# Kernel tuning notes

Hardware: AMD Instinct MI355X
Metric: run time of the kernel (lower is better)

Reference implementation:

```python
import jax, jax.numpy as jnp
import numpy as np

EPS_LAM = 1e-6
GN_GROUPS = 4
GN_EPS = 1e-5


def _conv(x, k):
    # x: (N, Cin, H, W), k: (Cout, Cin, 3, 3), SAME padding, stride 1
    return jax.lax.conv_general_dilated(x, k, (1, 1), 'SAME',
                                        dimension_numbers=('NCHW', 'OIHW', 'NCHW'))


def _clifford_conv(x, wa, wb, ba, bb):
    # Cl(0,1) (complex-style) Clifford conv: channels split into two blade components.
    C = x.shape[1]
    h = C // 2
    a, b = x[:, :h], x[:, h:]
    oa = _conv(a, wa) - _conv(b, wb) + ba[None, :, None, None]
    ob = _conv(a, wb) + _conv(b, wa) + bb[None, :, None, None]
    return jnp.concatenate([oa, ob], axis=1)


def _helmholtz(x):
    # Project the vector field (vx = first half of channels, vy = second half)
    # onto its divergence-free component in Fourier space.
    N, C, H, W = x.shape
    h = C // 2
    vx, vy = x[:, :h], x[:, h:]
    kx = jnp.fft.rfftfreq(W)[None, :]   # (1, FW)
    ky = jnp.fft.fftfreq(H)[:, None]    # (H, 1)
    k2 = kx * kx + ky * ky              # (H, FW)
    vxh = jnp.fft.rfft2(vx, norm='ortho')
    vyh = jnp.fft.rfft2(vy, norm='ortho')
    num = kx * vxh + ky * vyh
    p = jnp.where(k2 == 0, 0.0, num / jnp.where(k2 == 0, 1.0, k2))
    vxp = jnp.fft.irfft2(vxh - kx * p, s=(H, W), norm='ortho')
    vyp = jnp.fft.irfft2(vyh - ky * p, s=(H, W), norm='ortho')
    return jnp.concatenate([vxp, vyp], axis=1)


def _group_norm(x, w, b):
    N, C, H, W = x.shape
    xg = x.reshape(N, GN_GROUPS, -1)
    mu = xg.mean(-1, keepdims=True)
    var = xg.var(-1, keepdims=True)
    xn = ((xg - mu) * jax.lax.rsqrt(var + GN_EPS)).reshape(N, C, H, W)
    return xn * w[None, :, None, None] + b[None, :, None, None]


def setup_inputs() -> dict:
    key = jax.random.key(0)
    ks = jax.random.split(key, 6)
    B, T, C, H, W = 2, 16, 128, 64, 64
    hC = C // 2
    sc = 0.05
    return {
        'x_seq': jax.random.normal(ks[0], (B, T, C, H, W), jnp.float32),
        'dt_seq': jax.random.uniform(ks[1], (B, T), jnp.float32, 0.05, 1.0),
        'gen_w': jax.random.normal(ks[2], (C, 2 * C), jnp.float32) * (1.0 / np.sqrt(C)),
        'gen_b': jnp.zeros((2 * C,), jnp.float32),
        'cw_a': jax.random.normal(ks[3], (hC, hC, 3, 3), jnp.float32) * sc,
        'cw_b': jax.random.normal(ks[4], (hC, hC, 3, 3), jnp.float32) * sc,
        'cb_a': jnp.zeros((hC,), jnp.float32),
        'cb_b': jnp.zeros((hC,), jnp.float32),
        'gn_w': jnp.ones((C,), jnp.float32),
        'gn_b': jnp.zeros((C,), jnp.float32),
    }


def reference(x_seq, dt_seq, gen_w, gen_b, cw_a, cw_b, cb_a, cb_b, gn_w, gn_b):
    B, T, C, H, W = x_seq.shape
    dt = dt_seq[:, :, None, None, None]                   # (B,T,1,1,1)
    x_fft = jnp.fft.rfft2(x_seq, norm='ortho')            # (B,T,C,H,FW) complex64
    stats = x_seq.mean(axis=(-1, -2))                     # (B,T,C)
    params = stats @ gen_w + gen_b                        # (B,T,2C)
    nu, omega = jnp.split(params, 2, axis=-1)
    lam = (-jnp.abs(nu) + 1j * omega)[:, :, :, None, None]  # (B,T,C,1,1)
    A_scan = jnp.exp(lam * dt)
    small = jnp.abs(lam) < EPS_LAM
    safe = jnp.where(small, jnp.complex64(EPS_LAM), lam)
    X_term = jnp.where(small, dt.astype(jnp.complex64), (jnp.exp(safe * dt) - 1.0) / safe)
    X = (x_fft * X_term).astype(jnp.complex64)            # (B,T,C,H,FW)
    A = jnp.broadcast_to(A_scan.astype(jnp.complex64), X.shape)

    def comb(l, r):
        al, xl = l
        ar, xr = r
        return (al * ar, ar * xl + xr)

    _, h_fft = jax.lax.associative_scan(comb, (A, X), axis=1)  # h_t = A_t h_{t-1} + X_t
    h = jnp.fft.irfft2(h_fft, s=(H, W), norm='ortho')
    hf = h.reshape(B * T, C, H, W)
    u = hf + _clifford_conv(hf, cw_a, cw_b, cb_a, cb_b)
    u = _helmholtz(u)
    out = _group_norm(u, gn_w, gn_b)
    return out.reshape(B, T, C, H, W)
```

## Files before the change

kernel.cpp:

```cpp
#include <hip/hip_runtime.h>
#include <math.h>

#define PI_F 3.14159265358979323846f
#define ST 66

typedef __attribute__((ext_vector_type(8))) short short8;
typedef __attribute__((ext_vector_type(4))) float f32x4;
typedef __attribute__((ext_vector_type(4))) unsigned short u16x4;
typedef __attribute__((ext_vector_type(8))) unsigned short u16x8;
typedef __attribute__((ext_vector_type(4))) unsigned uint4v;

static __device__ __forceinline__ int sw(int row, int intra) {
    return row * ST + (intra ^ (row & 7));
}

static __device__ __forceinline__ unsigned short f2bf(float x) {
    unsigned u = __float_as_uint(x);
    unsigned r = (u + 0x7FFF + ((u >> 16) & 1)) >> 16;
    return (unsigned short)r;
}
static __device__ __forceinline__ float bf2f(unsigned short u) {
    return __uint_as_float(((unsigned)u) << 16);
}
static __device__ __forceinline__ float2 unpk(unsigned v) {
    return make_float2(bf2f((unsigned short)(v & 0xffff)), bf2f((unsigned short)(v >> 16)));
}

static __device__ __forceinline__ float2 cadd(float2 a, float2 b) { return make_float2(a.x + b.x, a.y + b.y); }
static __device__ __forceinline__ float2 csub(float2 a, float2 b) { return make_float2(a.x - b.x, a.y - b.y); }
static __device__ __forceinline__ float2 cmul(float2 a, float2 b) { return make_float2(a.x * b.x - a.y * b.y, a.x * b.y + a.y * b.x); }
static __device__ __forceinline__ float2 cmulc(float2 a, float2 b) { return make_float2(a.x * b.x + a.y * b.y, a.y * b.x - a.x * b.y); }

template <int S>
static __device__ __forceinline__ void dft8(float2* z) {
    const float RT = 0.70710678118654752440f;
    float2 ee0 = cadd(z[0], z[4]), ee1 = csub(z[0], z[4]);
    float2 eo0 = cadd(z[2], z[6]), eo1 = csub(z[2], z[6]);
    float2 oe0 = cadd(z[1], z[5]), oe1 = csub(z[1], z[5]);
    float2 oo0 = cadd(z[3], z[7]), oo1 = csub(z[3], z[7]);
    float2 ieo1 = make_float2(-S * eo1.y, S * eo1.x);
    float2 ioo1 = make_float2(-S * oo1.y, S * oo1.x);
    float2 E0 = cadd(ee0, eo0), E2 = csub(ee0, eo0);
    float2 E1 = cadd(ee1, ieo1), E3 = csub(ee1, ieo1);
    float2 O0 = cadd(oe0, oo0), O2 = csub(oe0, oo0);
    float2 O1 = cadd(oe1, ioo1), O3 = csub(oe1, ioo1);
    float2 w1O1 = make_float2(RT * (O1.x - S * O1.y), RT * (S * O1.x + O1.y));
    float2 w3O3 = make_float2(RT * (-O3.x - S * O3.y), RT * (S * O3.x - O3.y));
    float2 iO2  = make_float2(-S * O2.y, S * O2.x);
    z[0] = cadd(E0, O0);   z[4] = csub(E0, O0);
    z[1] = cadd(E1, w1O1); z[5] = csub(E1, w1O1);
    z[2] = cadd(E2, iO2);  z[6] = csub(E2, iO2);
    z[3] = cadd(E3, w3O3); z[7] = csub(E3, w3O3);
}

template <int S>
static __device__ __forceinline__ void fftRowsA(float2* G, const float2* twl, int tid) {
#pragma unroll
    for (int sl = 0; sl < 2; ++sl) {
        int s = tid + sl * 256;
        int row = s >> 3, b = s & 7;
        float2 z[8];
#pragma unroll
        for (int a = 0; a < 8; ++a) z[a] = G[sw(row, 8 * a + b)];
        dft8<S>(z);
#pragma unroll
        for (int c = 0; c < 8; ++c) {
            float2 t = twl[(b * c) & 63];
            G[sw(row, 8 * c + b)] = (S < 0) ? cmul(z[c], t) : cmulc(z[c], t);
        }
    }
}
template <int S>
static __device__ __forceinline__ void fftRowsB(float2* G, int tid) {
    int r0 = tid >> 3, c = tid & 7, r1 = r0 + 32;
    float2 z0[8], z1[8];
#pragma unroll
    for (int b = 0; b < 8; ++b) z0[b] = G[sw(r0, 8 * c + b)];
#pragma unroll
    for (int b = 0; b < 8; ++b) z1[b] = G[sw(r1, 8 * c + b)];
    dft8<S>(z0); dft8<S>(z1);
    __syncthreads();
#pragma unroll
    for (int d = 0; d < 8; ++d) G[sw(r0, c + 8 * d)] = z0[d];
#pragma unroll
    for (int d = 0; d < 8; ++d) G[sw(r1, c + 8 * d)] = z1[d];
}
template <int S>
static __device__ __forceinline__ void fftColsA(float2* G, const float2* twl, int tid) {
#pragma unroll
    for (int sl = 0; sl < 2; ++sl) {
        int s = tid + sl * 256;
        int col = s & 63, b = s >> 6;
        float2 z[8];
#pragma unroll
        for (int a = 0; a < 8; ++a) z[a] = G[sw(8 * a + b, col)];
        dft8<S>(z);
#pragma unroll
        for (int c = 0; c < 8; ++c) {
            float2 t = twl[(b * c) & 63];
            G[sw(8 * c + b, col)] = (S < 0) ? cmul(z[c], t) : cmulc(z[c], t);
        }
    }
}
template <int S>
static __device__ __forceinline__ void fftColsB(float2* G, int tid) {
    int col = tid & 63, c0 = tid >> 6, c1 = c0 + 4;
    float2 z0[8], z1[8];
#pragma unroll
    for (int b = 0; b < 8; ++b) z0[b] = G[sw(8 * c0 + b, col)];
#pragma unroll
    for (int b = 0; b < 8; ++b) z1[b] = G[sw(8 * c1 + b, col)];
    dft8<S>(z0); dft8<S>(z1);
    __syncthreads();
#pragma unroll
    for (int d = 0; d < 8; ++d) G[sw(c0 + 8 * d, col)] = z0[d];
#pragma unroll
    for (int d = 0; d < 8; ++d) G[sw(c1 + 8 * d, col)] = z1[d];
}

__global__ __launch_bounds__(256) void k_params(const float* __restrict__ stats,
                                                const float* __restrict__ gw,
                                                const float* __restrict__ gb,
                                                const float* __restrict__ dts,
                                                float2* __restrict__ A,
                                                float2* __restrict__ Xt) {
    int idx = blockIdx.x * 256 + threadIdx.x;
    int c = idx & 127;
    int bt = idx >> 7;
    const float* st = stats + bt * 128;
    float nu = gb[c], om = gb[c + 128];
    for (int k = 0; k < 128; ++k) {
        float s = st[k];
        nu += s * gw[k * 256 + c];
        om += s * gw[k * 256 + c + 128];
    }
    float dt = dts[bt];
    float lre = -fabsf(nu);
    float lim = om;
    float mag = sqrtf(lre * lre + lim * lim);
    float er = expf(lre * dt);
    float sn, cs;
    sincosf(lim * dt, &sn, &cs);
    float2 Av = make_float2(er * cs, er * sn);
    float2 X;
    if (mag < 1e-6f) {
        X = make_float2(dt, 0.f);
    } else {
        float ar = Av.x - 1.f, ai = Av.y;
        float inv = 1.f / (mag * mag);
        X = make_float2((ar * lre + ai * lim) * inv, (ai * lre - ar * lim) * inv);
    }
    A[idx] = Av;
    Xt[idx] = X;
}

__global__ __launch_bounds__(256) void k_rfft2s(const float* __restrict__ xin,
                                                unsigned* __restrict__ Sb,
                                                float* __restrict__ stats) {
    int p = blockIdx.x, tid = threadIdx.x;
    __shared__ float2 G[64 * ST], twl[64];
    __shared__ float red[8];
    if (tid < 64) {
        float sn, cs;
        sincosf(-(2.0f * PI_F / 64.0f) * (float)tid, &sn, &cs);
        twl[tid] = make_float2(cs, sn);
    }
    const float* x0 = xin + (size_t)(2 * p) * 4096;
    const float* x1 = x0 + 4096;
    float s0 = 0.f, s1 = 0.f;
    for (int i4 = tid; i4 < 1024; i4 += 256) {
        float4 a = ((const float4*)x0)[i4];
        float4 b = ((const float4*)x1)[i4];
        s0 += a.x + a.y + a.z + a.w;
        s1 += b.x + b.y + b.z + b.w;
        int r = i4 >> 4, w = (i4 & 15) << 2;
        G[sw(r, w + 0)] = make_float2(a.x, b.x);
        G[sw(r, w + 1)] = make_float2(a.y, b.y);
        G[sw(r, w + 2)] = make_float2(a.z, b.z);
        G[sw(r, w + 3)] = make_float2(a.w, b.w);
    }
    for (int off = 32; off > 0; off >>= 1) {
        s0 += __shfl_xor(s0, off, 64);
        s1 += __shfl_xor(s1, off, 64);
    }
    if ((tid & 63) == 0) { red[(tid >> 6) * 2] = s0; red[(tid >> 6) * 2 + 1] = s1; }
    __syncthreads();
    if (tid < 2) {
        float t = red[tid] + red[tid + 2] + red[tid + 4] + red[tid + 6];
        stats[2 * p + tid] = t * (1.0f / 4096.0f);
    }
    fftRowsA<-1>(G, twl, tid); __syncthreads();
    fftRowsB<-1>(G, tid);      __syncthreads();
    fftColsA<-1>(G, twl, tid); __syncthreads();
    fftColsB<-1>(G, tid);      __syncthreads();

    unsigned* o0 = Sb + (size_t)(2 * p) * 2112;
    unsigned* o1 = o0 + 2112;
    for (int i = tid; i < 2112; i += 256) {
        int my = i / 33, mx = i - my * 33;
        float2 Zk = G[sw(my, mx)];
        float2 Zm = G[sw((64 - my) & 63, (64 - mx) & 63)];
        float a0 = (Zk.x + Zm.x) * (0.5f / 64.0f);
        float a1 = (Zk.y - Zm.y) * (0.5f / 64.0f);
        float b0 = (Zk.y + Zm.y) * (0.5f / 64.0f);
        float b1 = (Zm.x - Zk.x) * (0.5f / 64.0f);
        o0[i] = (unsigned)f2bf(a0) | ((unsigned)f2bf(a1) << 16);
        o1[i] = (unsigned)f2bf(b0) | ((unsigned)f2bf(b1) << 16);
    }
}

__global__ __launch_bounds__(256) void k_scan(unsigned* __restrict__ Sb,
                                              const float2* __restrict__ A,
                                              const float2* __restrict__ Xt) {
    int tid = blockIdx.x * 256 + threadIdx.x;
    int s = tid % 528;
    int c = (tid / 528) & 127;
    int b = tid / (528 * 128);
    float2 h0 = make_float2(0.f, 0.f), h1 = h0, h2 = h0, h3 = h0;
    for (int t = 0; t < 16; ++t) {
        int bt = b * 16 + t;
        float2 a = A[bt * 128 + c];
        float2 xt = Xt[bt * 128 + c];
        size_t off = ((size_t)(bt * 128 + c)) * 2112 + 4 * s;
        uint4v v = *(uint4v*)(Sb + off);
        float2 x0 = cmul(unpk(v[0]), xt);
        float2 x1 = cmul(unpk(v[1]), xt);
        float2 x2 = cmul(unpk(v[2]), xt);
        float2 x3 = cmul(unpk(v[3]), xt);
        h0 = make_float2(a.x * h0.x - a.y * h0.y + x0.x, a.x * h0.y + a.y * h0.x + x0.y);
        h1 = make_float2(a.x * h1.x - a.y * h1.y + x1.x, a.x * h1.y + a.y * h1.x + x1.y);
        h2 = make_float2(a.x * h2.x - a.y * h2.y + x2.x, a.x * h2.y + a.y * h2.x + x2.y);
        h3 = make_float2(a.x * h3.x - a.y * h3.y + x3.x, a.x * h3.y + a.y * h3.x + x3.y);
        uint4v o;
        o[0] = (unsigned)f2bf(h0.x) | ((unsigned)f2bf(h0.y) << 16);
        o[1] = (unsigned)f2bf(h1.x) | ((unsigned)f2bf(h1.y) << 16);
        o[2] = (unsigned)f2bf(h2.x) | ((unsigned)f2bf(h2.y) << 16);
        o[3] = (unsigned)f2bf(h3.x) | ((unsigned)f2bf(h3.y) << 16);
        *(uint4v*)(Sb + off) = o;
    }
}

__global__ __launch_bounds__(256) void k_irfft2b(const unsigned* __restrict__ Sb,
                                                 unsigned short* __restrict__ hb) {
    int p = blockIdx.x, tid = threadIdx.x;
    __shared__ float2 G[64 * ST], twl[64];
    if (tid < 64) {
        float sn, cs;
        sincosf(-(2.0f * PI_F / 64.0f) * (float)tid, &sn, &cs);
        twl[tid] = make_float2(cs, sn);
    }
    const unsigned* i0 = Sb + (size_t)(2 * p) * 2112;
    const unsigned* i1 = i0 + 2112;
    for (int i = tid; i < 1984; i += 256) {
        int mx = 1 + i % 31, my = i / 31;
        int idx = my * 33 + mx;
        float2 a = unpk(i0[idx]);
        float2 b = unpk(i1[idx]);
        G[sw(my, mx)] = make_float2(a.x - b.y, a.y + b.x);
        G[sw((64 - my) & 63, 64 - mx)] = make_float2(a.x + b.y, b.x - a.y);
    }
    if (tid < 64) {
        int mx = (tid >= 32) ? 32 : 0;
        int r = tid & 31;
        if (r == 0) {
#pragma unroll
            for (int q = 0; q < 2; ++q) {
                int my = q * 32;
                float2 a = unpk(i0[my * 33 + mx]);
                float2 b = unpk(i1[my * 33 + mx]);
                G[sw(my, mx)] = make_float2(a.x, b.x);
            }
        } else {
            int my = r, my2 = 64 - r;
            float2 A0 = unpk(i0[my * 33 + mx]),  B0 = unpk(i0[my2 * 33 + mx]);
            float2 A1 = unpk(i1[my * 33 + mx]),  B1 = unpk(i1[my2 * 33 + mx]);
            float2 V0 = make_float2((A0.x + B0.x) * 0.5f, (A0.y - B0.y) * 0.5f);
            float2 V1 = make_float2((A1.x + B1.x) * 0.5f, (A1.y - B1.y) * 0.5f);
            G[sw(my, mx)]  = make_float2(V0.x - V1.y, V0.y + V1.x);
            G[sw(my2, mx)] = make_float2(V0.x + V1.y, V1.x - V0.y);
        }
    }
    __syncthreads();
    fftColsA<1>(G, twl, tid); __syncthreads();
    fftColsB<1>(G, tid);      __syncthreads();
    fftRowsA<1>(G, twl, tid); __syncthreads();
    fftRowsB<1>(G, tid);      __syncthreads();

    unsigned short* h0 = hb + (size_t)(2 * p) * 4096;
    unsigned short* h1 = h0 + 4096;
    for (int i4 = tid; i4 < 1024; i4 += 256) {
        int r = i4 >> 4, w = (i4 & 15) << 2;
        u16x4 oa, ob;
#pragma unroll
        for (int e = 0; e < 4; ++e) {
            float2 v = G[sw(r, w + e)];
            oa[e] = f2bf(v.x * (1.0f / 64.0f));
            ob[e] = f2bf(v.y * (1.0f / 64.0f));
        }
        ((u16x4*)h0)[i4] = oa;
        ((u16x4*)h1)[i4] = ob;
    }
}

__global__ __launch_bounds__(256) void k_wprep(const float* __restrict__ cwa,
                                               const float* __restrict__ cwb,
                                               unsigned short* __restrict__ Wb) {
    int idx = blockIdx.x * 256 + threadIdx.x;
    int kl = idx & 31;
    int m = (idx >> 5) & 127;
    int tcb = idx >> 12;
    int cb = tcb & 3, t = tcb >> 2;
    int ci = cb * 32 + kl;
    int mm = m & 63, cc = ci & 63;
    float w;
    if (m < 64) w = (ci < 64) ? cwa[(mm * 64 + cc) * 9 + t] : -cwb[(mm * 64 + cc) * 9 + t];
    else        w = (ci < 64) ? cwb[(mm * 64 + cc) * 9 + t] :  cwa[(mm * 64 + cc) * 9 + t];
    if (m == ci && t == 4) w += 1.0f;
    Wb[idx] = f2bf(w);
}

__global__ __launch_bounds__(256, 2) void k_conv_mfma(const unsigned short* __restrict__ hb,
                                                      const unsigned short* __restrict__ Wb,
                                                      const float* __restrict__ cba,
                                                      const float* __restrict__ cbb,
                                                      unsigned short* __restrict__ uout) {
    __shared__ __align__(16) char smem[65536];
    int f = blockIdx.y;
    int r0 = blockIdx.x * 2;
    int tid = threadIdx.x;
    const unsigned short* base = hb + (size_t)f * 524288;

    int wid = tid >> 6, lane = tid & 63;
    int lhi = lane >> 4, llo = lane & 15;
    int row_off = wid & 1;
    int mbase = (wid >> 1) * 64;

    auto ldA = [&](int it, short8* a) {
        const unsigned short* wp = Wb + ((size_t)(it * 128 + mbase + llo)) * 32 + lhi * 8;
#pragma unroll
        for (int mf = 0; mf < 4; ++mf) a[mf] = *(const short8*)(wp + mf * 16 * 32);
    };
    auto ldB = [&](int it, short8* b) {
        int t = it >> 2, cb = it & 3;
        int dy = t / 3 - 1, dx = t % 3 - 1;
        int prow = row_off + 1 + dy;
        int slot = cb * 4 + lhi;
#pragma unroll
        for (int nf = 0; nf < 4; ++nf) {
            int c = nf * 16 + llo;
            int cdx = c + dx;
            bool valid = ((unsigned)cdx < 64u);
            int cr = valid ? cdx : c;
            int byteoff = ((prow * 64 + cr) << 8) + ((slot ^ (cr & 15)) << 4);
            short8 bb = *(const short8*)(smem + byteoff);
            b[nf] = valid ? bb : (short8)0;
        }
    };

    short8 aC[4], aN[4], aN2[4], bC[4], bN[4];
    ldA(0, aC);
    ldA(1, aN);

    for (int j = tid; j < 4096; j += 256) {
        int row = j >> 10;
        int cig = (j >> 6) & 15;
        int col = j & 63;
        int gr = r0 - 1 + row;
        short8 v = (short8)0;
        if ((unsigned)gr < 64u) {
            const unsigned short* p = base + (size_t)(cig * 8) * 4096 + gr * 64 + col;
#pragma unroll
            for (int e = 0; e < 8; ++e) v[e] = (short)p[(size_t)e * 4096];
        }
        int byteoff = ((row * 64 + col) << 8) + ((cig ^ (col & 15)) << 4);
        *(short8*)(smem + byteoff) = v;
    }
    __syncthreads();

    f32x4 acc[4][4];
#pragma unroll
    for (int mf = 0; mf < 4; ++mf)
#pragma unroll
        for (int nf = 0; nf < 4; ++nf) acc[mf][nf] = (f32x4)0.f;

    ldB(0, bC);
#pragma unroll
    for (int it = 0; it < 36; ++it) {
        if (it < 34) ldA(it + 2, aN2);
        if (it < 35) ldB(it + 1, bN);
        __builtin_amdgcn_s_setprio(1);
#pragma unroll
        for (int mf = 0; mf < 4; ++mf)
#pragma unroll
            for (int nf = 0; nf < 4; ++nf)
                acc[mf][nf] = __builtin_amdgcn_mfma_f32_16x16x32_bf16(aC[mf], bC[nf], acc[mf][nf], 0, 0, 0);
        __builtin_amdgcn_s_setprio(0);
#pragma unroll
        for (int k = 0; k < 4; ++k) { aC[k] = aN[k]; aN[k] = aN2[k]; bC[k] = bN[k]; }
    }

    int grow = r0 + row_off;
#pragma unroll
    for (int mf = 0; mf < 4; ++mf) {
#pragma unroll
        for (int r = 0; r < 4; ++r) {
            int co = mbase + mf * 16 + lhi * 4 + r;
            float bias = (co < 64) ? cba[co] : cbb[co - 64];
            unsigned short* op = uout + ((size_t)f * 128 + co) * 4096 + (size_t)grow * 64;
#pragma unroll
            for (int nf = 0; nf < 4; ++nf)
                op[nf * 16 + llo] = f2bf(acc[mf][nf][r] + bias);
        }
    }
}

__global__ __launch_bounds__(256) void k_helm(const unsigned short* __restrict__ uin,
                                              unsigned short* __restrict__ uo,
                                              float* __restrict__ partials) {
    int bid = blockIdx.x;
    int f = bid >> 6, c = bid & 63;
    int tid = threadIdx.x;
    __shared__ float2 G[64 * ST], twl[64];
    __shared__ float red[16];
    if (tid < 64) {
        float sn, cs;
        sincosf(-(2.0f * PI_F / 64.0f) * (float)tid, &sn, &cs);
        twl[tid] = make_float2(cs, sn);
    }
    const unsigned short* u0 = uin + ((size_t)f * 128 + c) * 4096;
    const unsigned short* u1 = u0 + (size_t)64 * 4096;
    for (int i4 = tid; i4 < 1024; i4 += 256) {
        u16x4 a = ((const u16x4*)u0)[i4];
        u16x4 b = ((const u16x4*)u1)[i4];
        int r = i4 >> 4, w = (i4 & 15) << 2;
#pragma unroll
        for (int e = 0; e < 4; ++e)
            G[sw(r, w + e)] = make_float2(bf2f(a[e]), bf2f(b[e]));
    }
    __syncthreads();
    fftRowsA<-1>(G, twl, tid); __syncthreads();
    fftRowsB<-1>(G, tid);      __syncthreads();
    fftColsA<-1>(G, twl, tid); __syncthreads();
    fftColsB<-1>(G, tid);      __syncthreads();

    for (int i = tid; i < 1984; i += 256) {
        int mx = 1 + i % 31, my = i / 31;
        float2 Zk = G[sw(my, mx)];
        float2 Zm = G[sw((64 - my) & 63, 64 - mx)];
        float2 Vx = make_float2((Zk.x + Zm.x) * 0.5f, (Zk.y - Zm.y) * 0.5f);
        float2 Vy = make_float2((Zk.y + Zm.y) * 0.5f, (Zm.x - Zk.x) * 0.5f);
        float fx = (float)mx * (1.0f / 64.0f);
        float fy = (float)(my < 32 ? my : my - 64) * (1.0f / 64.0f);
        float inv = 1.0f / (fx * fx + fy * fy);
        float Pr = (fx * Vx.x + fy * Vy.x) * inv;
        float Pi = (fx * Vx.y + fy * Vy.y) * inv;
        Vx.x -= fx * Pr; Vx.y -= fx * Pi;
        Vy.x -= fy * Pr; Vy.y -= fy * Pi;
        G[sw(my, mx)] = make_float2(Vx.x - Vy.y, Vx.y + Vy.x);
        G[sw((64 - my) & 63, 64 - mx)] = make_float2(Vx.x + Vy.y, Vy.x - Vx.y);
    }
    if (tid < 64) {
        int mx = (tid >= 32) ? 32 : 0;
        int r = tid & 31;
        float fx = (float)mx * (1.0f / 64.0f);
        if (r == 0) {
#pragma unroll
            for (int q = 0; q < 2; ++q) {
                int my = q * 32;
                float fy = (my == 0) ? 0.f : -0.5f;
                float k2 = fx * fx + fy * fy;
                float2 Z = G[sw(my, mx)];
                float vx = Z.x, vy = Z.y;
                if (k2 > 0.f) {
                    float P = (fx * vx + fy * vy) / k2;
                    vx -= fx * P; vy -= fy * P;
                }
                G[sw(my, mx)] = make_float2(vx, vy);
            }
        } else {
            int my = r, my2 = 64 - r;
            float fy = (float)my * (1.0f / 64.0f);
            float inv = 1.0f / (fx * fx + fy * fy);
            float2 Zk = G[sw(my, mx)];
            float2 Zm = G[sw(my2, mx)];
            float2 Vx = make_float2((Zk.x + Zm.x) * 0.5f, (Zk.y - Zm.y) * 0.5f);
            float2 Vy = make_float2((Zk.y + Zm.y) * 0.5f, (Zm.x - Zk.x) * 0.5f);
            float Pr = (fx * Vx.x + fy * Vy.x) * inv;
            float Pi = (fx * Vx.y + fy * Vy.y) * inv;
            float2 Xk = make_float2(Vx.x - fx * Pr, Vx.y - fx * Pi);
            float2 Yk = make_float2(Vy.x - fy * Pr, Vy.y - fy * Pi);
            float P2r = (fx * Vx.x - fy * Vy.x) * inv;
            float P2i = (-fx * Vx.y + fy * Vy.y) * inv;
            float2 Xk2 = make_float2(Vx.x - fx * P2r, -Vx.y - fx * P2i);
            float2 Yk2 = make_float2(Vy.x + fy * P2r, -Vy.y + fy * P2i);
            float2 Xh = make_float2((Xk.x + Xk2.x) * 0.5f, (Xk.y - Xk2.y) * 0.5f);
            float2 Yh = make_float2((Yk.x + Yk2.x) * 0.5f, (Yk.y - Yk2.y) * 0.5f);
            G[sw(my, mx)]  = make_float2(Xh.x - Yh.y, Xh.y + Yh.x);
            G[sw(my2, mx)] = make_float2(Xh.x + Yh.y, Yh.x - Xh.y);
        }
    }
    __syncthreads();
    fftColsA<1>(G, twl, tid); __syncthreads();
    fftColsB<1>(G, tid);      __syncthreads();
    fftRowsA<1>(G, twl, tid); __syncthreads();
    fftRowsB<1>(G, tid);      __syncthreads();

    unsigned short* o0 = uo + ((size_t)f * 128 + c) * 4096;
    unsigned short* o1 = o0 + (size_t)64 * 4096;
    float s0 = 0.f, q0 = 0.f, s1 = 0.f, q1 = 0.f;
    for (int i4 = tid; i4 < 1024; i4 += 256) {
        int r = i4 >> 4, w = (i4 & 15) << 2;
        u16x4 oa, ob;
#pragma unroll
        for (int e = 0; e < 4; ++e) {
            float2 v = G[sw(r, w + e)];
            float a = v.x * (1.0f / 4096.0f);
            float b = v.y * (1.0f / 4096.0f);
            s0 += a; q0 += a * a; s1 += b; q1 += b * b;
            oa[e] = f2bf(a); ob[e] = f2bf(b);
        }
        ((u16x4*)o0)[i4] = oa;
        ((u16x4*)o1)[i4] = ob;
    }
    for (int off = 32; off > 0; off >>= 1) {
        s0 += __shfl_xor(s0, off, 64); q0 += __shfl_xor(q0, off, 64);
        s1 += __shfl_xor(s1, off, 64); q1 += __shfl_xor(q1, off, 64);
    }
    if ((tid & 63) == 0) {
        int w6 = tid >> 6;
        red[w6 * 4 + 0] = s0; red[w6 * 4 + 1] = q0;
        red[w6 * 4 + 2] = s1; red[w6 * 4 + 3] = q1;
    }
    __syncthreads();
    if (tid == 0) {
        float S0 = 0.f, Q0 = 0.f, S1 = 0.f, Q1 = 0.f;
#pragma unroll
        for (int w6 = 0; w6 < 4; ++w6) {
            S0 += red[w6 * 4 + 0]; Q0 += red[w6 * 4 + 1];
            S1 += red[w6 * 4 + 2]; Q1 += red[w6 * 4 + 3];
        }
        float* pp = partials + ((size_t)f * 64 + c) * 4;
        pp[0] = S0; pp[1] = Q0; pp[2] = S1; pp[3] = Q1;
    }
}

__global__ __launch_bounds__(128) void k_gnfin(const float* __restrict__ partials,
                                               float2* __restrict__ gs) {
    int i = threadIdx.x;
    int f = i >> 2, g = i & 3;
    const float4* p4 = (const float4*)partials;
    float s = 0.f, q = 0.f;
    if (g < 2) {
        for (int cc = 0; cc < 32; ++cc) {
            float4 p = p4[f * 64 + g * 32 + cc];
            s += p.x; q += p.y;
        }
    } else {
        for (int cc = 0; cc < 32; ++cc) {
            float4 p = p4[f * 64 + (g - 2) * 32 + cc];
            s += p.z; q += p.w;
        }
    }
    float mu = s * (1.0f / 131072.0f);
    float var = q * (1.0f / 131072.0f) - mu * mu;
    gs[i] = make_float2(mu, rsqrtf(var + 1e-5f));
}

__global__ __launch_bounds__(256) void k_gnapply(const unsigned short* __restrict__ u,
                                                 const float2* __restrict__ gs,
                                                 const float* __restrict__ gnw,
                                                 const float* __restrict__ gnb,
                                                 float* __restrict__ out) {
    size_t i8 = (size_t)blockIdx.x * 256 + threadIdx.x;
    u16x8 v = ((const u16x8*)u)[i8];
    int cl = (int)(i8 >> 9);
    int c = cl & 127;
    int fg = cl >> 5;
    float2 ms = gs[fg];
    float sc = ms.y * gnw[c];
    float sh = gnb[c] - ms.x * sc;
    float4 r0, r1;
    r0.x = bf2f(v[0]) * sc + sh; r0.y = bf2f(v[1]) * sc + sh;
    r0.z = bf2f(v[2]) * sc + sh; r0.w = bf2f(v[3]) * sc + sh;
    r1.x = bf2f(v[4]) * sc + sh; r1.y = bf2f(v[5]) * sc + sh;
    r1.z = bf2f(v[6]) * sc + sh; r1.w = bf2f(v[7]) * sc + sh;
    ((float4*)out)[i8 * 2]     = r0;
    ((float4*)out)[i8 * 2 + 1] = r1;
}

extern "C" void kernel_launch(void* const* d_in, const int* in_sizes, int n_in,
                              void* d_out, int out_size, void* d_ws, size_t ws_size,
                              hipStream_t stream) {
    (void)in_sizes; (void)n_in; (void)out_size; (void)ws_size;
    const float* x   = (const float*)d_in[0];
    const float* dts = (const float*)d_in[1];
    const float* gw  = (const float*)d_in[2];
    const float* gb  = (const float*)d_in[3];
    const float* cwa = (const float*)d_in[4];
    const float* cwb = (const float*)d_in[5];
    const float* cba = (const float*)d_in[6];
    const float* cbb = (const float*)d_in[7];
    const float* gnw = (const float*)d_in[8];
    const float* gnb = (const float*)d_in[9];
    float* out = (float*)d_out;
    char* ws = (char*)d_ws;

    unsigned*       Sb  = (unsigned*)ws;
    unsigned short* Hb  = (unsigned short*)(ws + 34603008);
    unsigned short* Ub  = (unsigned short*)(ws + 68157440);
    unsigned short* H1b = (unsigned short*)(ws + 101711872);
    float*  stats    = (float*)(ws + 135266304);
    float2* A        = (float2*)(ws + 135282688);
    float2* Xt       = (float2*)(ws + 135315456);
    float2* gs       = (float2*)(ws + 135348224);
    float*  partials = (float*)(ws + 135349248);
    unsigned short* Wb = (unsigned short*)ws;

    k_rfft2s<<<2048, 256, 0, stream>>>(x, Sb, stats);
    k_params<<<16, 256, 0, stream>>>(stats, gw, gb, dts, A, Xt);
    k_scan<<<528, 256, 0, stream>>>(Sb, A, Xt);
    k_irfft2b<<<2048, 256, 0, stream>>>(Sb, Hb);
    k_wprep<<<576, 256, 0, stream>>>(cwa, cwb, Wb);
    k_conv_mfma<<<dim3(32, 32), 256, 0, stream>>>(Hb, Wb, cba, cbb, Ub);
    k_helm<<<2048, 256, 0, stream>>>(Ub, H1b, partials);
    k_gnfin<<<1, 128, 0, stream>>>(partials, gs);
    k_gnapply<<<8192, 256, 0, stream>>>(H1b, gs, gnw, gnb, out);
}
```

Baseline: 210.0 us.

## Store irfft output channel-last so conv loads 16-byte vectors

The inverse FFT kernel now writes its bf16 result in a channel-innermost (HWC) layout, packing the two channels it handles into one 32-bit store with a 256-byte stride. The conv kernel's shared-memory fill then reads eight contiguous channels as a single 16-byte load instead of eight strided 2-byte gathers. This trades coalesced writes in the irfft kernel for strided 4-byte scatters, in exchange for much more efficient reads in the conv kernel.

```diff
diff --git a/kernel.cpp b/kernel.cpp
--- a/kernel.cpp
+++ b/kernel.cpp
@@ -241,7 +241,7 @@
 }
 
 __global__ __launch_bounds__(256) void k_irfft2b(const unsigned* __restrict__ Sb,
-                                                 unsigned short* __restrict__ hb) {
+                                                 unsigned short* __restrict__ hc) {
     int p = blockIdx.x, tid = threadIdx.x;
     __shared__ float2 G[64 * ST], twl[64];
     if (tid < 64) {
@@ -286,19 +286,15 @@
     fftRowsA<1>(G, twl, tid); __syncthreads();
     fftRowsB<1>(G, tid);      __syncthreads();
 
-    unsigned short* h0 = hb + (size_t)(2 * p) * 4096;
-    unsigned short* h1 = h0 + 4096;
-    for (int i4 = tid; i4 < 1024; i4 += 256) {
-        int r = i4 >> 4, w = (i4 & 15) << 2;
-        u16x4 oa, ob;
-#pragma unroll
-        for (int e = 0; e < 4; ++e) {
-            float2 v = G[sw(r, w + e)];
-            oa[e] = f2bf(v.x * (1.0f / 64.0f));
-            ob[e] = f2bf(v.y * (1.0f / 64.0f));
-        }
-        ((u16x4*)h0)[i4] = oa;
-        ((u16x4*)h1)[i4] = ob;
+    int f = (2 * p) >> 7;
+    int c0 = (2 * p) & 127;
+    unsigned short* hb = hc + (size_t)f * 524288 + c0;
+    for (int i = tid; i < 4096; i += 256) {
+        int r = i >> 6, col = i & 63;
+        float2 v = G[sw(r, col)];
+        unsigned pk = (unsigned)f2bf(v.x * (1.0f / 64.0f)) |
+                      ((unsigned)f2bf(v.y * (1.0f / 64.0f)) << 16);
+        *(unsigned*)(hb + (size_t)i * 128) = pk;
     }
 }
 
@@ -319,7 +315,7 @@
     Wb[idx] = f2bf(w);
 }
 
-__global__ __launch_bounds__(256, 2) void k_conv_mfma(const unsigned short* __restrict__ hb,
+__global__ __launch_bounds__(256, 2) void k_conv_mfma(const unsigned short* __restrict__ hc,
                                                       const unsigned short* __restrict__ Wb,
                                                       const float* __restrict__ cba,
                                                       const float* __restrict__ cbb,
@@ -328,7 +324,7 @@
     int f = blockIdx.y;
     int r0 = blockIdx.x * 2;
     int tid = threadIdx.x;
-    const unsigned short* base = hb + (size_t)f * 524288;
+    const unsigned short* base = hc + (size_t)f * 524288;
 
     int wid = tid >> 6, lane = tid & 63;
     int lhi = lane >> 4, llo = lane & 15;
@@ -363,15 +359,12 @@
 
     for (int j = tid; j < 4096; j += 256) {
         int row = j >> 10;
-        int cig = (j >> 6) & 15;
-        int col = j & 63;
+        int col = (j >> 4) & 63;
+        int cig = j & 15;
         int gr = r0 - 1 + row;
         short8 v = (short8)0;
-        if ((unsigned)gr < 64u) {
-            const unsigned short* p = base + (size_t)(cig * 8) * 4096 + gr * 64 + col;
-#pragma unroll
-            for (int e = 0; e < 8; ++e) v[e] = (short)p[(size_t)e * 4096];
-        }
+        if ((unsigned)gr < 64u)
+            v = *(const short8*)(base + ((size_t)(gr * 64 + col)) * 128 + cig * 8);
         int byteoff = ((row * 64 + col) << 8) + ((cig ^ (col & 15)) << 4);
         *(short8*)(smem + byteoff) = v;
     }
@@ -606,7 +599,7 @@
     char* ws = (char*)d_ws;
 
     unsigned*       Sb  = (unsigned*)ws;
-    unsigned short* Hb  = (unsigned short*)(ws + 34603008);
+    unsigned short* Hc  = (unsigned short*)(ws + 34603008);
     unsigned short* Ub  = (unsigned short*)(ws + 68157440);
     unsigned short* H1b = (unsigned short*)(ws + 101711872);
     float*  stats    = (float*)(ws + 135266304);
@@ -619,9 +612,9 @@
     k_rfft2s<<<2048, 256, 0, stream>>>(x, Sb, stats);
     k_params<<<16, 256, 0, stream>>>(stats, gw, gb, dts, A, Xt);
     k_scan<<<528, 256, 0, stream>>>(Sb, A, Xt);
-    k_irfft2b<<<2048, 256, 0, stream>>>(Sb, Hb);
+    k_irfft2b<<<2048, 256, 0, stream>>>(Sb, Hc);
     k_wprep<<<576, 256, 0, stream>>>(cwa, cwb, Wb);
-    k_conv_mfma<<<dim3(32, 32), 256, 0, stream>>>(Hb, Wb, cba, cbb, Ub);
+    k_conv_mfma<<<dim3(32, 32), 256, 0, stream>>>(Hc, Wb, cba, cbb, Ub);
     k_helm<<<2048, 256, 0, stream>>>(Ub, H1b, partials);
     k_gnfin<<<1, 128, 0, stream>>>(partials, gs);
     k_gnapply<<<8192, 256, 0, stream>>>(H1b, gs, gnw, gnb, out);
```

Result: slower. 250.6 us (+19.4%).
